# Performance work log

Measured on AMD Instinct MI355X. Metric: run time of the kernel, lower is better.

Reference implementation:

```python
import jax, jax.numpy as jnp
import numpy as np

B, C, Hf, Wf, HM, P = 64, 2048, 16, 16, 256, 10  # P = num_parts, NP = graph nodes
NP = P - 1
EPS = 1e-5  # BatchNorm eps

def bn_eval(x, g, b, rm, rv):
    return (x - rm) * jax.lax.rsqrt(rv + EPS) * g + b

def setup_inputs() -> dict:
    key = jax.random.key(0)
    ks = jax.random.split(key, 6)
    return {
        "x_global": jax.random.normal(ks[0], (B, C, Hf, Wf), jnp.float32),
        "x_gcn": jax.random.normal(ks[1], (B, C, Hf, Wf), jnp.float32),
        "mask": jax.random.randint(ks[2], (B, 1, HM, HM), 0, P, jnp.int32),
        "adj": jax.random.uniform(ks[3], (B, NP, NP), jnp.float32),
        "W1": jax.random.normal(ks[4], (C, C), jnp.float32) * 0.02,
        "b1": jnp.zeros((C,), jnp.float32),
        "g1": jnp.ones((NP * C,), jnp.float32), "be1": jnp.zeros((NP * C,), jnp.float32),
        "rm1": jnp.zeros((NP * C,), jnp.float32), "rv1": jnp.ones((NP * C,), jnp.float32),
        "W2": jax.random.normal(ks[5], (C, C), jnp.float32) * 0.02,
        "b2": jnp.zeros((C,), jnp.float32),
        "g2": jnp.ones((NP * C,), jnp.float32), "be2": jnp.zeros((NP * C,), jnp.float32),
        "rm2": jnp.zeros((NP * C,), jnp.float32), "rv2": jnp.ones((NP * C,), jnp.float32),
        "gb_g": jnp.ones((C,), jnp.float32), "gb_b": jnp.zeros((C,), jnp.float32),
        "gb_rm": jnp.zeros((C,), jnp.float32), "gb_rv": jnp.ones((C,), jnp.float32),
        "gn_g": jnp.ones((C,), jnp.float32), "gn_b": jnp.zeros((C,), jnp.float32),
        "gn_rm": jnp.zeros((C,), jnp.float32), "gn_rv": jnp.ones((C,), jnp.float32),
    }

def gc_layer(x, adj, Wt, bias, g, be, rm, rv):
    # GraphConvolution: matmul -> bmm(adj) -> bias -> BN over flattened (B, NP*C)
    s = jnp.einsum('bpc,cd->bpd', x, Wt)
    o = jnp.einsum('bpq,bqd->bpd', adj, s) + bias
    flat = o.reshape(o.shape[0], -1)
    return bn_eval(flat, g, be, rm, rv).reshape(o.shape)

def reference(x_global, x_gcn, mask, adj, W1, b1, g1, be1, rm1, rv1,
              W2, b2, g2, be2, rm2, rv2, gb_g, gb_b, gb_rm, gb_rv,
              gn_g, gn_b, gn_rm, gn_rv):
    # --- global branch: GAP + bottleneck BN (eval) ---
    feat_global = x_global.mean(axis=(2, 3))                      # (B, C)
    bnfeat_global = bn_eval(feat_global, gb_g, gb_b, gb_rm, gb_rv)

    # --- nearest-neighbor downsample of mask to feature-map size ---
    stride = HM // Hf
    mr = mask[:, 0, ::stride, ::stride]                           # (B, h, w)

    # one-hot part masks for classes 1..P-1: (B, h, w, NP)
    onehot = (mr[..., None] == jnp.arange(1, P)).astype(jnp.float32)
    counts = onehot.sum(axis=(1, 2))                              # (B, NP)

    # deterministic part dropout: drop the first present part per image
    drop = jnp.argmax(counts > 0, axis=1) + 1                     # (B,)
    keep = (mr != drop[:, None, None]).astype(jnp.float32)        # (B, h, w)
    x_self = x_gcn * keep[:, None, :, :]

    # segment mean pooling per part: (B, NP, C)
    denom = (counts + 1e-8)[..., None]
    mask_feat = jnp.einsum('bchw,bhwp->bpc', x_gcn, onehot) / denom
    self_feat = jnp.einsum('bchw,bhwp->bpc', x_self, onehot) / denom

    def gcn(x):
        x1 = jax.nn.relu(gc_layer(x, adj, W1, b1, g1, be1, rm1, rv1))
        x2 = jax.nn.relu(gc_layer(x1, adj, W2, b2, g2, be2, rm2, rv2))
        return x2.mean(axis=1), x2.reshape(x2.shape[0], -1)

    feat_gcn, feat_gcn_cat = gcn(mask_feat)
    feat_self, feat_self_cat = gcn(self_feat)
    bnfeat_gcn = bn_eval(feat_gcn, gn_g, gn_b, gn_rm, gn_rv)
    bnfeat_self = bn_eval(feat_self, gn_g, gn_b, gn_rm, gn_rv)

    # concatenate eval-mode outputs into one array: (B, 3*C + 2*NP*C)
    return jnp.concatenate([bnfeat_global, bnfeat_gcn, bnfeat_self,
                            feat_gcn_cat, feat_self_cat], axis=1)
```

## Files before the change

kernel.cpp:

```cpp
#include <hip/hip_runtime.h>
#include <cstdint>
#include <cstddef>

#define EPSV 1e-5f
#define GK 2048

typedef __bf16 bf16x8 __attribute__((ext_vector_type(8)));
typedef float f32x4 __attribute__((ext_vector_type(4)));

__device__ __forceinline__ unsigned short f2bf(float f) {
  unsigned int u = __float_as_uint(f);
  u += 0x7FFFu + ((u >> 16) & 1u);
  return (unsigned short)(u >> 16);
}

__device__ __forceinline__ void async_copy16(const void* src, void* dst_lds) {
  __builtin_amdgcn_global_load_lds(
      (const __attribute__((address_space(1))) void*)src,
      (__attribute__((address_space(3))) void*)dst_lds, 16, 0, 0);
}

__global__ __launch_bounds__(256) void pool(
    const float* __restrict__ x, const int* __restrict__ mask,
    unsigned short* __restrict__ Abuf) {
  __shared__ unsigned char pid8[256];
  __shared__ int cnt[10];
  const int t = threadIdx.x;
  const int b = blockIdx.x >> 5;
  const int c0 = (blockIdx.x & 31) * 64;

  int m = mask[(size_t)b * 65536 + (t >> 4) * 4096 + (t & 15) * 16];
  if (t < 10) cnt[t] = 0;
  __syncthreads();
  atomicAdd(&cnt[m], 1);
  pid8[t] = (unsigned char)m;
  __syncthreads();

  const int w = t >> 6;
  const int l16 = t & 15;
  const int quad = (t & 63) >> 4;
  const float* xrow = x + ((size_t)(b * 2048 + c0 + w * 16 + l16)) * 256;
  const unsigned int tgt = (unsigned int)(l16 + 1);

  f32x4 acc = (f32x4){0.f, 0.f, 0.f, 0.f};
#pragma unroll
  for (int ks = 0; ks < 8; ks++) {
    const float4 va = *(const float4*)(xrow + ks * 32 + quad * 8);
    const float4 vb = *(const float4*)(xrow + ks * 32 + quad * 8 + 4);
    uint2 pc = *(const uint2*)&pid8[ks * 32 + quad * 8];
    union { bf16x8 v; unsigned int u[4]; } bfr;
#pragma unroll
    for (int d = 0; d < 4; d++) {
      unsigned int word = (d < 2) ? pc.x : pc.y;
      unsigned int sh = (d & 1) * 16;
      unsigned int b0 = (word >> sh) & 0xFFu;
      unsigned int b1 = (word >> (sh + 8)) & 0xFFu;
      bfr.u[d] = (b0 == tgt ? 0x3F80u : 0u) | (b1 == tgt ? 0x3F800000u : 0u);
    }
    bf16x8 af;
    af[0] = (__bf16)va.x; af[1] = (__bf16)va.y;
    af[2] = (__bf16)va.z; af[3] = (__bf16)va.w;
    af[4] = (__bf16)vb.x; af[5] = (__bf16)vb.y;
    af[6] = (__bf16)vb.z; af[7] = (__bf16)vb.w;
    acc = __builtin_amdgcn_mfma_f32_16x16x32_bf16(af, bfr.v, acc, 0, 0, 0);
  }

  if (l16 < 9) {
    const int p = l16;
    float invp = 1.f / ((float)cnt[p + 1] + 1e-8f);
    int dm1 = 0;
#pragma unroll
    for (int q = 8; q >= 0; q--)
      if (cnt[q + 1] > 0) dm1 = q;
    int cbase = c0 + w * 16 + quad * 4;
    ushort4 hm;
    hm.x = f2bf(acc[0] * invp);
    hm.y = f2bf(acc[1] * invp);
    hm.z = f2bf(acc[2] * invp);
    hm.w = f2bf(acc[3] * invp);
    ushort4 hs = (p == dm1) ? (ushort4){0, 0, 0, 0} : hm;
    *(ushort4*)&Abuf[(size_t)(b * 9 + p) * 2048 + cbase] = hm;
    *(ushort4*)&Abuf[(size_t)((64 + b) * 9 + p) * 2048 + cbase] = hs;
  }
}

__global__ __launch_bounds__(256) void prep(
    const float* __restrict__ W1, const float* __restrict__ W2,
    unsigned short* __restrict__ Wt1, unsigned short* __restrict__ Wt2,
    const float* __restrict__ xg, const float* __restrict__ gb_g,
    const float* __restrict__ gb_b, const float* __restrict__ gb_rm,
    const float* __restrict__ gb_rv, float* __restrict__ out,
    const float* __restrict__ b1, const float* __restrict__ g1,
    const float* __restrict__ be1, const float* __restrict__ rm1,
    const float* __restrict__ rv1, const float* __restrict__ b2,
    const float* __restrict__ g2, const float* __restrict__ be2,
    const float* __restrict__ rm2, const float* __restrict__ rv2,
    float* __restrict__ sc1, float* __restrict__ sh1,
    float* __restrict__ sc2, float* __restrict__ sh2) {
  __shared__ float tile[32][33];
  const int blk = blockIdx.x;
  const int t = threadIdx.x;

  if (blk < 8192) {
    int z = blk >> 12;
    int rem = blk & 4095;
    int by = rem >> 6, bx = rem & 63;
    const float* W = z ? W2 : W1;
    unsigned short* Wt = z ? Wt2 : Wt1;
    int tx = t & 31;
    int ty = t >> 5;
    int k0 = by * 32, n0 = bx * 32;
#pragma unroll
    for (int i = 0; i < 32; i += 8)
      tile[ty + i][tx] = W[(size_t)(k0 + ty + i) * 2048 + n0 + tx];
    __syncthreads();
#pragma unroll
    for (int i = 0; i < 32; i += 8)
      Wt[(size_t)(n0 + ty + i) * 2048 + k0 + tx] = f2bf(tile[tx][ty + i]);
  } else if (blk < 16384) {
    int base = (blk - 8192) * 16 + (t >> 6) * 4;
    int lane = t & 63;
    const float4* xp = (const float4*)xg + (size_t)base * 64 + lane;
    float4 v0 = xp[0], v1 = xp[64], v2 = xp[128], v3 = xp[192];
    float s0 = v0.x + v0.y + v0.z + v0.w;
    float s1 = v1.x + v1.y + v1.z + v1.w;
    float s2 = v2.x + v2.y + v2.z + v2.w;
    float s3 = v3.x + v3.y + v3.z + v3.w;
#pragma unroll
    for (int o = 32; o > 0; o >>= 1) {
      s0 += __shfl_xor(s0, o, 64);
      s1 += __shfl_xor(s1, o, 64);
      s2 += __shfl_xor(s2, o, 64);
      s3 += __shfl_xor(s3, o, 64);
    }
    if (lane == 0) {
      int b = base >> 11, c = base & 2047;
      float mm[4] = {s0 * (1.f / 256.f), s1 * (1.f / 256.f),
                     s2 * (1.f / 256.f), s3 * (1.f / 256.f)};
      float4 o4;
      float* po = &o4.x;
#pragma unroll
      for (int r = 0; r < 4; r++) {
        int cc = c + r;
        po[r] = (mm[r] - gb_rm[cc]) / sqrtf(gb_rv[cc] + EPSV) * gb_g[cc] +
                gb_b[cc];
      }
      *(float4*)(out + (size_t)b * 43008 + c) = o4;
    }
  } else {
    int i = (blk - 16384) * 256 + t;
    int z = i >= 18432;
    int f = i - z * 18432;
    int d = f & 2047;
    const float* g = z ? g2 : g1;
    const float* be = z ? be2 : be1;
    const float* rm = z ? rm2 : rm1;
    const float* rv = z ? rv2 : rv1;
    const float* bias = z ? b2 : b1;
    float sc = g[f] / sqrtf(rv[f] + EPSV);
    float sh = (bias[d] - rm[f]) * sc + be[f];
    (z ? sc2 : sc1)[f] = sc;
    (z ? sh2 : sh1)[f] = sh;
  }
}

#define SPART (1152 * 2048)
__global__ __launch_bounds__(256) void gemm_db(
    const unsigned short* __restrict__ A, const unsigned short* __restrict__ Bt,
    float* __restrict__ S) {
  __shared__ unsigned short As[2][128 * 64];
  __shared__ unsigned short Bs[2][64 * 64];
  const int tid = threadIdx.x;
  const int lane = tid & 63;
  const int wave = tid >> 6;
  const int wm = (wave >> 1) << 6;
  const int wn = (wave & 1) << 5;
  const int quad = lane >> 4;
  const int l16 = lane & 15;
  const int by = blockIdx.y;
  const int bx = blockIdx.x;
  const int kz = blockIdx.z;

  const unsigned short* Ag = A + (size_t)by * 128 * GK;
  const unsigned short* Bg = Bt + (size_t)bx * 64 * GK;
  S += (size_t)kz * SPART;

  f32x4 acc[4][2];
#pragma unroll
  for (int i = 0; i < 4; i++)
#pragma unroll
    for (int j = 0; j < 2; j++) acc[i][j] = (f32x4){0.f, 0.f, 0.f, 0.f};

  int srA[4], scA[4];
#pragma unroll
  for (int s = 0; s < 4; s++) {
    int idx = tid + s * 256;
    srA[s] = idx >> 3;
    scA[s] = ((idx & 7) ^ (srA[s] & 7)) * 8;
  }
  int srB[2], scB[2];
#pragma unroll
  for (int s = 0; s < 2; s++) {
    int idx = tid + s * 256;
    srB[s] = idx >> 3;
    scB[s] = ((idx & 7) ^ (srB[s] & 7)) * 8;
  }

  const int kbeg = kz * 1024;

#define STAGE(buf, kk)                                                        \
  do {                                                                        \
    _Pragma("unroll") for (int s = 0; s < 4; s++) {                           \
      int idx = tid + s * 256;                                                \
      async_copy16(Ag + (size_t)srA[s] * GK + (kk) + scA[s],                  \
                   &As[buf][idx * 8]);                                        \
    }                                                                         \
    _Pragma("unroll") for (int s = 0; s < 2; s++) {                           \
      int idx = tid + s * 256;                                                \
      async_copy16(Bg + (size_t)srB[s] * GK + (kk) + scB[s],                  \
                   &Bs[buf][idx * 8]);                                        \
    }                                                                         \
  } while (0)

  STAGE(0, kbeg);
  asm volatile("s_waitcnt vmcnt(0)" ::: "memory");
  __syncthreads();

  for (int it = 0; it < 16; it++) {
    const int cur = it & 1;
    if (it < 15) STAGE(cur ^ 1, kbeg + (it + 1) * 64);

#pragma unroll
    for (int ks = 0; ks < 2; ks++) {
      bf16x8 af[4], bfr[2];
#pragma unroll
      for (int i = 0; i < 4; i++) {
        int row = wm + i * 16 + l16;
        int slot = row * 8 + ((ks * 4 + quad) ^ (row & 7));
        af[i] = *(const bf16x8*)&As[cur][slot * 8];
      }
#pragma unroll
      for (int j = 0; j < 2; j++) {
        int row = wn + j * 16 + l16;
        int slot = row * 8 + ((ks * 4 + quad) ^ (row & 7));
        bfr[j] = *(const bf16x8*)&Bs[cur][slot * 8];
      }
#pragma unroll
      for (int i = 0; i < 4; i++)
#pragma unroll
        for (int j = 0; j < 2; j++)
          acc[i][j] = __builtin_amdgcn_mfma_f32_16x16x32_bf16(
              af[i], bfr[j], acc[i][j], 0, 0, 0);
    }

    if (it < 15) {
      asm volatile("s_waitcnt vmcnt(0)" ::: "memory");
      __syncthreads();
    }
  }
#undef STAGE

#pragma unroll
  for (int i = 0; i < 4; i++)
#pragma unroll
    for (int j = 0; j < 2; j++)
#pragma unroll
      for (int r = 0; r < 4; r++) {
        int m = by * 128 + wm + i * 16 + quad * 4 + r;
        int n = bx * 64 + wn + j * 16 + l16;
        S[(size_t)m * 2048 + n] = acc[i][j][r];
      }
}

__global__ __launch_bounds__(256) void epi_mid(
    const float* __restrict__ S, const float* __restrict__ adj,
    const float* __restrict__ sc, const float* __restrict__ sh,
    unsigned short* __restrict__ Aout) {
  int idx = blockIdx.x * 256 + threadIdx.x;
  int d = idx & 2047;
  int bb = idx >> 11;
  int b = bb & 63;
  float s[9];
#pragma unroll
  for (int q = 0; q < 9; q++) {
    size_t off = (size_t)(bb * 9 + q) * 2048 + d;
    s[q] = S[off] + S[off + SPART];
  }
#pragma unroll
  for (int p = 0; p < 9; p++) {
    float o = 0.f;
#pragma unroll
    for (int q = 0; q < 9; q++) o += adj[b * 81 + p * 9 + q] * s[q];
    int f = p * 2048 + d;
    float v = fmaxf(o * sc[f] + sh[f], 0.f);
    Aout[(size_t)(bb * 9 + p) * 2048 + d] = f2bf(v);
  }
}

__global__ __launch_bounds__(256) void epi_final(
    const float* __restrict__ S, const float* __restrict__ adj,
    const float* __restrict__ sc, const float* __restrict__ sh,
    const float* __restrict__ gn_g, const float* __restrict__ gn_b,
    const float* __restrict__ gn_rm, const float* __restrict__ gn_rv,
    float* __restrict__ out) {
  int idx = blockIdx.x * 256 + threadIdx.x;
  int d = idx & 2047;
  int bb = idx >> 11;
  int b = bb & 63;
  bool selfb = bb >= 64;
  float s[9];
#pragma unroll
  for (int q = 0; q < 9; q++) {
    size_t off = (size_t)(bb * 9 + q) * 2048 + d;
    s[q] = S[off] + S[off + SPART];
  }
  float* orow = out + (size_t)b * 43008;
  size_t catbase = selfb ? 24576 : 6144;
  float mean = 0.f;
#pragma unroll
  for (int p = 0; p < 9; p++) {
    float o = 0.f;
#pragma unroll
    for (int q = 0; q < 9; q++) o += adj[b * 81 + p * 9 + q] * s[q];
    int f = p * 2048 + d;
    float v = fmaxf(o * sc[f] + sh[f], 0.f);
    mean += v;
    orow[catbase + f] = v;
  }
  mean *= (1.f / 9.f);
  orow[(selfb ? 4096 : 2048) + d] =
      (mean - gn_rm[d]) / sqrtf(gn_rv[d] + EPSV) * gn_g[d] + gn_b[d];
}

extern "C" void kernel_launch(void* const* d_in, const int* in_sizes, int n_in,
                              void* d_out, int out_size, void* d_ws,
                              size_t ws_size, hipStream_t stream) {
  const float* x_global = (const float*)d_in[0];
  const float* x_gcn = (const float*)d_in[1];
  const int* mask = (const int*)d_in[2];
  const float* adj = (const float*)d_in[3];
  const float* W1 = (const float*)d_in[4];
  const float* b1 = (const float*)d_in[5];
  const float* g1 = (const float*)d_in[6];
  const float* be1 = (const float*)d_in[7];
  const float* rm1 = (const float*)d_in[8];
  const float* rv1 = (const float*)d_in[9];
  const float* W2 = (const float*)d_in[10];
  const float* b2 = (const float*)d_in[11];
  const float* g2 = (const float*)d_in[12];
  const float* be2 = (const float*)d_in[13];
  const float* rm2 = (const float*)d_in[14];
  const float* rv2 = (const float*)d_in[15];
  const float* gb_g = (const float*)d_in[16];
  const float* gb_b = (const float*)d_in[17];
  const float* gb_rm = (const float*)d_in[18];
  const float* gb_rv = (const float*)d_in[19];
  const float* gn_g = (const float*)d_in[20];
  const float* gn_b = (const float*)d_in[21];
  const float* gn_rm = (const float*)d_in[22];
  const float* gn_rv = (const float*)d_in[23];
  float* out = (float*)d_out;

  char* ws = (char*)d_ws;
  unsigned short* Abuf = (unsigned short*)(ws);
  unsigned short* Wt1 = (unsigned short*)(ws + 4718592);
  unsigned short* Wt2 = (unsigned short*)(ws + 13107200);
  float* S = (float*)(ws + 21495808);
  float* sc1 = (float*)(ws + 40370176);
  float* sh1 = (float*)(ws + 40443904);
  float* sc2 = (float*)(ws + 40517632);
  float* sh2 = (float*)(ws + 40591360);

  pool<<<2048, 256, 0, stream>>>(x_gcn, mask, Abuf);
  prep<<<16528, 256, 0, stream>>>(W1, W2, Wt1, Wt2, x_global, gb_g, gb_b,
                                  gb_rm, gb_rv, out, b1, g1, be1, rm1, rv1,
                                  b2, g2, be2, rm2, rv2, sc1, sh1, sc2, sh2);
  gemm_db<<<dim3(32, 9, 2), 256, 0, stream>>>(Abuf, Wt1, S);
  epi_mid<<<1024, 256, 0, stream>>>(S, adj, sc1, sh1, Abuf);
  gemm_db<<<dim3(32, 9, 2), 256, 0, stream>>>(Abuf, Wt2, S);
  epi_final<<<1024, 256, 0, stream>>>(S, adj, sc2, sh2, gn_g, gn_b, gn_rm,
                                      gn_rv, out);
}
```

Baseline: 410.2 us.

## Derive self-branch first GEMM from mask branch via linearity; split prep kernel

The self features equal the mask features with one part row zeroed. Their first-layer product is therefore the mask product with that row's contribution removed. The first GEMM now runs only on the 576 mask rows, and epi_mid builds the self branch by subtracting adj[p,drop]*S[drop] before bias/BN/ReLU. The drop index is written per image by pool. The combined prep kernel is split into separate transpose, mean-BN and fold kernels, which adds launches. The M tiling (5 blocks of 128 covering 576 rows) needs a row guard on the S stores, and the last tile reads Abuf rows past 576 that are ignored.

```diff
diff --git a/kernel.cpp b/kernel.cpp
--- a/kernel.cpp
+++ b/kernel.cpp
@@ -22,7 +22,7 @@
 
 __global__ __launch_bounds__(256) void pool(
     const float* __restrict__ x, const int* __restrict__ mask,
-    unsigned short* __restrict__ Abuf) {
+    unsigned short* __restrict__ Abuf, int* __restrict__ dropm1) {
   __shared__ unsigned char pid8[256];
   __shared__ int cnt[10];
   const int t = threadIdx.x;
@@ -68,28 +68,82 @@
   if (l16 < 9) {
     const int p = l16;
     float invp = 1.f / ((float)cnt[p + 1] + 1e-8f);
-    int dm1 = 0;
-#pragma unroll
-    for (int q = 8; q >= 0; q--)
-      if (cnt[q + 1] > 0) dm1 = q;
     int cbase = c0 + w * 16 + quad * 4;
     ushort4 hm;
     hm.x = f2bf(acc[0] * invp);
     hm.y = f2bf(acc[1] * invp);
     hm.z = f2bf(acc[2] * invp);
     hm.w = f2bf(acc[3] * invp);
-    ushort4 hs = (p == dm1) ? (ushort4){0, 0, 0, 0} : hm;
     *(ushort4*)&Abuf[(size_t)(b * 9 + p) * 2048 + cbase] = hm;
-    *(ushort4*)&Abuf[(size_t)((64 + b) * 9 + p) * 2048 + cbase] = hs;
-  }
-}
-
-__global__ __launch_bounds__(256) void prep(
+  }
+  if (t == 0 && (blockIdx.x & 31) == 0) {
+    int dp = 0;
+    for (int p = 8; p >= 0; p--)
+      if (cnt[p + 1] > 0) dp = p;
+    dropm1[b] = dp;
+  }
+}
+
+__global__ __launch_bounds__(256) void transp(
     const float* __restrict__ W1, const float* __restrict__ W2,
-    unsigned short* __restrict__ Wt1, unsigned short* __restrict__ Wt2,
+    unsigned short* __restrict__ Wt1, unsigned short* __restrict__ Wt2) {
+  __shared__ float tile[32][33];
+  const int blk = blockIdx.x;
+  const int t = threadIdx.x;
+  int z = blk >> 12;
+  int rem = blk & 4095;
+  int by = rem >> 6, bx = rem & 63;
+  const float* W = z ? W2 : W1;
+  unsigned short* Wt = z ? Wt2 : Wt1;
+  int tx = t & 31;
+  int ty = t >> 5;
+  int k0 = by * 32, n0 = bx * 32;
+#pragma unroll
+  for (int i = 0; i < 32; i += 8)
+    tile[ty + i][tx] = W[(size_t)(k0 + ty + i) * 2048 + n0 + tx];
+  __syncthreads();
+#pragma unroll
+  for (int i = 0; i < 32; i += 8)
+    Wt[(size_t)(n0 + ty + i) * 2048 + k0 + tx] = f2bf(tile[tx][ty + i]);
+}
+
+__global__ __launch_bounds__(256) void meanbn(
     const float* __restrict__ xg, const float* __restrict__ gb_g,
     const float* __restrict__ gb_b, const float* __restrict__ gb_rm,
-    const float* __restrict__ gb_rv, float* __restrict__ out,
+    const float* __restrict__ gb_rv, float* __restrict__ out) {
+  const int w = threadIdx.x >> 6;
+  const int lane = threadIdx.x & 63;
+  const int base = blockIdx.x * 32 + w * 8;
+  const float4* xp = (const float4*)xg + (size_t)base * 64 + lane;
+  float s[8];
+#pragma unroll
+  for (int r = 0; r < 8; r++) {
+    float4 v = xp[r * 64];
+    s[r] = v.x + v.y + v.z + v.w;
+  }
+#pragma unroll
+  for (int o = 32; o > 0; o >>= 1) {
+#pragma unroll
+    for (int r = 0; r < 8; r++) s[r] += __shfl_xor(s[r], o, 64);
+  }
+  if (lane == 0) {
+    int b = base >> 11, c = base & 2047;
+    float po[8];
+#pragma unroll
+    for (int r = 0; r < 8; r++) {
+      int cc = c + r;
+      po[r] = (s[r] * (1.f / 256.f) - gb_rm[cc]) / sqrtf(gb_rv[cc] + EPSV) *
+                  gb_g[cc] +
+              gb_b[cc];
+    }
+    float4 o4a = {po[0], po[1], po[2], po[3]};
+    float4 o4b = {po[4], po[5], po[6], po[7]};
+    *(float4*)(out + (size_t)b * 43008 + c) = o4a;
+    *(float4*)(out + (size_t)b * 43008 + c + 4) = o4b;
+  }
+}
+
+__global__ __launch_bounds__(256) void fold(
     const float* __restrict__ b1, const float* __restrict__ g1,
     const float* __restrict__ be1, const float* __restrict__ rm1,
     const float* __restrict__ rv1, const float* __restrict__ b2,
@@ -97,77 +151,25 @@
     const float* __restrict__ rm2, const float* __restrict__ rv2,
     float* __restrict__ sc1, float* __restrict__ sh1,
     float* __restrict__ sc2, float* __restrict__ sh2) {
-  __shared__ float tile[32][33];
-  const int blk = blockIdx.x;
-  const int t = threadIdx.x;
-
-  if (blk < 8192) {
-    int z = blk >> 12;
-    int rem = blk & 4095;
-    int by = rem >> 6, bx = rem & 63;
-    const float* W = z ? W2 : W1;
-    unsigned short* Wt = z ? Wt2 : Wt1;
-    int tx = t & 31;
-    int ty = t >> 5;
-    int k0 = by * 32, n0 = bx * 32;
-#pragma unroll
-    for (int i = 0; i < 32; i += 8)
-      tile[ty + i][tx] = W[(size_t)(k0 + ty + i) * 2048 + n0 + tx];
-    __syncthreads();
-#pragma unroll
-    for (int i = 0; i < 32; i += 8)
-      Wt[(size_t)(n0 + ty + i) * 2048 + k0 + tx] = f2bf(tile[tx][ty + i]);
-  } else if (blk < 16384) {
-    int base = (blk - 8192) * 16 + (t >> 6) * 4;
-    int lane = t & 63;
-    const float4* xp = (const float4*)xg + (size_t)base * 64 + lane;
-    float4 v0 = xp[0], v1 = xp[64], v2 = xp[128], v3 = xp[192];
-    float s0 = v0.x + v0.y + v0.z + v0.w;
-    float s1 = v1.x + v1.y + v1.z + v1.w;
-    float s2 = v2.x + v2.y + v2.z + v2.w;
-    float s3 = v3.x + v3.y + v3.z + v3.w;
-#pragma unroll
-    for (int o = 32; o > 0; o >>= 1) {
-      s0 += __shfl_xor(s0, o, 64);
-      s1 += __shfl_xor(s1, o, 64);
-      s2 += __shfl_xor(s2, o, 64);
-      s3 += __shfl_xor(s3, o, 64);
-    }
-    if (lane == 0) {
-      int b = base >> 11, c = base & 2047;
-      float mm[4] = {s0 * (1.f / 256.f), s1 * (1.f / 256.f),
-                     s2 * (1.f / 256.f), s3 * (1.f / 256.f)};
-      float4 o4;
-      float* po = &o4.x;
-#pragma unroll
-      for (int r = 0; r < 4; r++) {
-        int cc = c + r;
-        po[r] = (mm[r] - gb_rm[cc]) / sqrtf(gb_rv[cc] + EPSV) * gb_g[cc] +
-                gb_b[cc];
-      }
-      *(float4*)(out + (size_t)b * 43008 + c) = o4;
-    }
-  } else {
-    int i = (blk - 16384) * 256 + t;
-    int z = i >= 18432;
-    int f = i - z * 18432;
-    int d = f & 2047;
-    const float* g = z ? g2 : g1;
-    const float* be = z ? be2 : be1;
-    const float* rm = z ? rm2 : rm1;
-    const float* rv = z ? rv2 : rv1;
-    const float* bias = z ? b2 : b1;
-    float sc = g[f] / sqrtf(rv[f] + EPSV);
-    float sh = (bias[d] - rm[f]) * sc + be[f];
-    (z ? sc2 : sc1)[f] = sc;
-    (z ? sh2 : sh1)[f] = sh;
-  }
+  int i = blockIdx.x * 256 + threadIdx.x;
+  int z = i >= 18432;
+  int f = i - z * 18432;
+  int d = f & 2047;
+  const float* g = z ? g2 : g1;
+  const float* be = z ? be2 : be1;
+  const float* rm = z ? rm2 : rm1;
+  const float* rv = z ? rv2 : rv1;
+  const float* bias = z ? b2 : b1;
+  float sc = g[f] / sqrtf(rv[f] + EPSV);
+  float sh = (bias[d] - rm[f]) * sc + be[f];
+  (z ? sc2 : sc1)[f] = sc;
+  (z ? sh2 : sh1)[f] = sh;
 }
 
 #define SPART (1152 * 2048)
 __global__ __launch_bounds__(256) void gemm_db(
     const unsigned short* __restrict__ A, const unsigned short* __restrict__ Bt,
-    float* __restrict__ S) {
+    float* __restrict__ S, int mlimit) {
   __shared__ unsigned short As[2][128 * 64];
   __shared__ unsigned short Bs[2][64 * 64];
   const int tid = threadIdx.x;
@@ -268,32 +270,36 @@
       for (int r = 0; r < 4; r++) {
         int m = by * 128 + wm + i * 16 + quad * 4 + r;
         int n = bx * 64 + wn + j * 16 + l16;
-        S[(size_t)m * 2048 + n] = acc[i][j][r];
+        if (m < mlimit) S[(size_t)m * 2048 + n] = acc[i][j][r];
       }
 }
 
 __global__ __launch_bounds__(256) void epi_mid(
     const float* __restrict__ S, const float* __restrict__ adj,
-    const float* __restrict__ sc, const float* __restrict__ sh,
-    unsigned short* __restrict__ Aout) {
+    const int* __restrict__ dropm1, const float* __restrict__ sc,
+    const float* __restrict__ sh, unsigned short* __restrict__ Aout) {
   int idx = blockIdx.x * 256 + threadIdx.x;
   int d = idx & 2047;
-  int bb = idx >> 11;
-  int b = bb & 63;
+  int b = idx >> 11;
   float s[9];
 #pragma unroll
   for (int q = 0; q < 9; q++) {
-    size_t off = (size_t)(bb * 9 + q) * 2048 + d;
+    size_t off = (size_t)(b * 9 + q) * 2048 + d;
     s[q] = S[off] + S[off + SPART];
   }
+  int dm1 = dropm1[b];
+  float sd = s[dm1];
 #pragma unroll
   for (int p = 0; p < 9; p++) {
     float o = 0.f;
 #pragma unroll
     for (int q = 0; q < 9; q++) o += adj[b * 81 + p * 9 + q] * s[q];
+    float os = o - adj[b * 81 + p * 9 + dm1] * sd;
     int f = p * 2048 + d;
-    float v = fmaxf(o * sc[f] + sh[f], 0.f);
-    Aout[(size_t)(bb * 9 + p) * 2048 + d] = f2bf(v);
+    float scv = sc[f], shv = sh[f];
+    Aout[(size_t)(b * 9 + p) * 2048 + d] = f2bf(fmaxf(o * scv + shv, 0.f));
+    Aout[(size_t)((64 + b) * 9 + p) * 2048 + d] =
+        f2bf(fmaxf(os * scv + shv, 0.f));
   }
 }
 
@@ -370,14 +376,16 @@
   float* sh1 = (float*)(ws + 40443904);
   float* sc2 = (float*)(ws + 40517632);
   float* sh2 = (float*)(ws + 40591360);
-
-  pool<<<2048, 256, 0, stream>>>(x_gcn, mask, Abuf);
-  prep<<<16528, 256, 0, stream>>>(W1, W2, Wt1, Wt2, x_global, gb_g, gb_b,
-                                  gb_rm, gb_rv, out, b1, g1, be1, rm1, rv1,
-                                  b2, g2, be2, rm2, rv2, sc1, sh1, sc2, sh2);
-  gemm_db<<<dim3(32, 9, 2), 256, 0, stream>>>(Abuf, Wt1, S);
-  epi_mid<<<1024, 256, 0, stream>>>(S, adj, sc1, sh1, Abuf);
-  gemm_db<<<dim3(32, 9, 2), 256, 0, stream>>>(Abuf, Wt2, S);
+  int* dropm1 = (int*)(ws + 40665088);
+
+  pool<<<2048, 256, 0, stream>>>(x_gcn, mask, Abuf, dropm1);
+  transp<<<8192, 256, 0, stream>>>(W1, W2, Wt1, Wt2);
+  meanbn<<<4096, 256, 0, stream>>>(x_global, gb_g, gb_b, gb_rm, gb_rv, out);
+  fold<<<144, 256, 0, stream>>>(b1, g1, be1, rm1, rv1, b2, g2, be2, rm2, rv2,
+                                sc1, sh1, sc2, sh2);
+  gemm_db<<<dim3(32, 5, 2), 256, 0, stream>>>(Abuf, Wt1, S, 576);
+  epi_mid<<<512, 256, 0, stream>>>(S, adj, dropm1, sc1, sh1, Abuf);
+  gemm_db<<<dim3(32, 9, 2), 256, 0, stream>>>(Abuf, Wt2, S, 1152);
   epi_final<<<1024, 256, 0, stream>>>(S, adj, sc2, sh2, gn_g, gn_b, gn_rm,
                                       gn_rv, out);
 }
```

Measured after the change: 410.5 us. No clear change (+0.1%).
